# Optimization experiments

Hardware: AMD Instinct MI355X
Metric: run time of the kernel (lower is better)

The kernel has to match this reference:

```python
import jax, jax.numpy as jnp
import numpy as np

B, NT, NZ, NX, NREC = 4, 256, 192, 192, 128
DT, DH = 0.001, 10.0


def setup_inputs() -> dict:
    key = jax.random.key(0)
    k1, k2, k3, k4 = jax.random.split(key, 4)
    # source wavelets, one trace per shot
    x = jax.random.normal(k1, (B, NT, 1), dtype=jnp.float32) * 1e2
    # realistic elastic media
    vp = 2500.0 + 1000.0 * jax.random.uniform(k2, (NZ, NX), dtype=jnp.float32)
    vs = vp / 1.78
    rho = 2000.0 + 300.0 * jax.random.uniform(k3, (NZ, NX), dtype=jnp.float32)
    # per-shot source location (z=5 near surface, random x)
    src_x = jax.random.randint(k4, (B,), 10, NX - 10)
    src_loc = jnp.stack([jnp.full((B,), 5), src_x], axis=1).astype(jnp.int32)
    # receiver line at depth z=5
    rec_x = jnp.linspace(10, NX - 10, NREC).astype(jnp.int32)
    rec_loc = jnp.stack([jnp.full((NREC,), 5, dtype=jnp.int32), rec_x], axis=1)
    return {"x": x, "vp": vp, "vs": vs, "rho": rho,
            "src_loc": src_loc, "rec_loc": rec_loc}


# staggered-grid first differences (forward / backward), zero-padded at edges
def _dxf(f):
    return jnp.pad(jnp.diff(f, axis=-1), ((0, 0), (0, 0), (0, 1))) / DH

def _dxb(f):
    return jnp.pad(jnp.diff(f, axis=-1), ((0, 0), (0, 0), (1, 0))) / DH

def _dzf(f):
    return jnp.pad(jnp.diff(f, axis=-2), ((0, 0), (0, 1), (0, 0))) / DH

def _dzb(f):
    return jnp.pad(jnp.diff(f, axis=-2), ((0, 0), (1, 0), (0, 0))) / DH


def _propagate(x, vp, vs, rho, src_loc, rec_loc):
    lam = rho * (vp ** 2 - 2.0 * vs ** 2)
    mu = rho * vs ** 2
    lam2mu = lam + 2.0 * mu
    buoy = DT / rho  # buoyancy * dt
    bidx = jnp.arange(B)
    sz, sx = src_loc[:, 0], src_loc[:, 1]
    rz, rx = rec_loc[:, 0], rec_loc[:, 1]

    def step(carry, wav_t):
        vx, vz, txx, tzz, txz = carry
        # velocity update from stress divergence
        vx = vx + buoy * (_dxf(txx) + _dzb(txz))
        vz = vz + buoy * (_dxb(txz) + _dzf(tzz))
        # stress update from velocity gradients
        dvxdx = _dxb(vx)
        dvzdz = _dzb(vz)
        txx = txx + DT * (lam2mu * dvxdx + lam * dvzdz)
        tzz = tzz + DT * (lam * dvxdx + lam2mu * dvzdz)
        txz = txz + DT * mu * (_dzf(vx) + _dxf(vz))
        # explosive source injection into txx, tzz (source_type = ['txx','tzz'])
        txx = txx.at[bidx, sz, sx].add(wav_t)
        tzz = tzz.at[bidx, sz, sx].add(wav_t)
        # probe extraction: (B, NREC)
        return (vx, vz, txx, tzz, txz), (vx[:, rz, rx], vz[:, rz, rx])

    z = jnp.zeros((B, NZ, NX), dtype=vp.dtype)
    _, (rvx, rvz) = jax.lax.scan(step, (z, z, z, z, z), x[:, :, 0].T)
    # torch: stack(dim=1) -> (B,NT,NREC); permute(1,2,0) -> (NT,NREC,B); cat dim=2
    y_vx = jnp.transpose(rvx, (0, 2, 1))  # (NT, NREC, B)
    y_vz = jnp.transpose(rvz, (0, 2, 1))
    return jnp.concatenate([y_vx, y_vz], axis=2)  # (NT, NREC, 2B)


def reference(x, vp, vs, rho, src_loc, rec_loc):
    return _propagate(x, vp, vs, rho, src_loc, rec_loc)
```

## Files before the change

### kernel.cpp

```cpp
#include <hip/hip_runtime.h>

#pragma clang fp contract(off)

#define B_    4
#define NT_   256
#define NZ_   192
#define NX_   192
#define NREC_ 128
#define DT_   0.001f
#define DH_   10.0f

#define N_CELL  (NZ_ * NX_)
#define N_FIELD (B_ * N_CELL)

#define K_     4
#define ROWS   3
#define NTHR   1024
#define VH     (2 * K_ - 1)
#define SH     (2 * K_)
#define VROWS  (ROWS + 2 * VH)
#define SROWS  (ROWS + 2 * SH)
#define TILES  (NZ_ / ROWS)
#define NBLK   (B_ * TILES)
#define NX4    (NX_ / 4)
#define LDS_BYTES ((2 * VROWS + 3 * SROWS) * NX_ * 4)

using f4 = __attribute__((ext_vector_type(4))) float;

__global__ void mat_kernel(const float* __restrict__ vp, const float* __restrict__ vs,
                           const float* __restrict__ rho,
                           float* __restrict__ lam, float* __restrict__ dtmu,
                           float* __restrict__ lam2mu, float* __restrict__ buoy) {
    int i = blockIdx.x * blockDim.x + threadIdx.x;
    if (i >= N_CELL) return;
    float vpi = vp[i], vsi = vs[i], rhoi = rho[i];
    float vs2 = vsi * vsi;
    float mui = rhoi * vs2;
    float lami = rhoi * (vpi * vpi - 2.0f * vs2);
    lam[i] = lami;
    dtmu[i] = DT_ * mui;
    lam2mu[i] = lami + 2.0f * mui;
    buoy[i] = DT_ * (1.0f / rhoi);
    buoy[i] = DT_ / rhoi;
}

template<int S>
__device__ __forceinline__ void substep(
    bool zin, int z, int srow, int x4, int x0, int z0, int sz, int sx, int b, int t0,
    f4& r_vx, f4& r_vz, f4& r_txx, f4& r_tzz, f4& r_txz,
    const f4& m_bu, const f4& m_l, const f4& m_lm, const f4& m_dtm,
    float* __restrict__ vxl, float* __restrict__ vzl,
    float* __restrict__ txxl, float* __restrict__ tzzl, float* __restrict__ txzl,
    const float* __restrict__ wav,
    bool rec_ok, int rec_idx, int tid, float* __restrict__ out,
    int base, float* __restrict__ vxw, float* __restrict__ vzw,
    float* __restrict__ txxw, float* __restrict__ tzzw, float* __restrict__ txzw) {
    const int t = t0 + S;
    const int sOff = srow * NX_ + x0;
    const int vOff = (srow - 1) * NX_ + x0;

    {
        constexpr int hv = 2 * (K_ - 1 - S) + 1;
        bool act = zin && (z >= z0 - hv) && (z <= z0 + ROWS - 1 + hv);
        if (act) {
            f4 txn  = *reinterpret_cast<const f4*>(txxl + sOff + (x4 < NX4 - 1 ? 4 : 0));
            f4 tzp  = *reinterpret_cast<const f4*>(txzl + sOff - (x4 > 0 ? 4 : 0));
            f4 tzm  = *reinterpret_cast<const f4*>(txzl + sOff - NX_);
            f4 tzzp = *reinterpret_cast<const f4*>(tzzl + sOff + NX_);
#pragma unroll
            for (int e = 0; e < 4; ++e) {
                int xg = x0 + e;
                float txx_c = r_txx[e];
                float txxp1 = (e == 3) ? txn[0] : r_txx[e + 1];
                float txz_c = r_txz[e];
                float txzm1 = (e == 0) ? tzp[3] : r_txz[e - 1];
                float dxf_txx = (xg < NX_ - 1) ? (txxp1 - txx_c) / DH_ : 0.0f;
                float dzb_txz = (z >= 1)       ? (txz_c - tzm[e]) / DH_ : 0.0f;
                float dxb_txz = (xg >= 1)      ? (txz_c - txzm1) / DH_ : 0.0f;
                float dzf_tzz = (z < NZ_ - 1)  ? (tzzp[e] - r_tzz[e]) / DH_ : 0.0f;
                r_vx[e] = r_vx[e] + m_bu[e] * (dxf_txx + dzb_txz);
                r_vz[e] = r_vz[e] + m_bu[e] * (dxb_txz + dzf_tzz);
            }
            *reinterpret_cast<f4*>(vxl + vOff) = r_vx;
            *reinterpret_cast<f4*>(vzl + vOff) = r_vz;
            if (S == K_ - 1) {
                if (z >= z0 && z < z0 + ROWS) {
                    *reinterpret_cast<f4*>(vxw + base + z * NX_ + x0) = r_vx;
                    *reinterpret_cast<f4*>(vzw + base + z * NX_ + x0) = r_vz;
                }
            }
        }
    }
    __syncthreads();

    if (rec_ok) {
        size_t o = ((size_t)t * NREC_ + tid) * (2 * B_);
        out[o + b]      = vxl[rec_idx];
        out[o + B_ + b] = vzl[rec_idx];
    }

    {
        constexpr int hs = 2 * (K_ - 1 - S);
        bool act = zin && (z >= z0 - hs) && (z <= z0 + ROWS - 1 + hs);
        if (act) {
            f4 vxp  = *reinterpret_cast<const f4*>(vxl + vOff - (x4 > 0 ? 4 : 0));
            f4 vxzp = *reinterpret_cast<const f4*>(vxl + vOff + NX_);
            f4 vzn  = *reinterpret_cast<const f4*>(vzl + vOff + (x4 < NX4 - 1 ? 4 : 0));
            f4 vzm  = *reinterpret_cast<const f4*>(vzl + vOff - NX_);
            float w = wav[b * NT_ + t];
#pragma unroll
            for (int e = 0; e < 4; ++e) {
                int xg = x0 + e;
                float vx_c = r_vx[e];
                float vz_c = r_vz[e];
                float vxm1 = (e == 0) ? vxp[3] : r_vx[e - 1];
                float vzp1 = (e == 3) ? vzn[0] : r_vz[e + 1];
                float dvxdx  = (xg >= 1)      ? (vx_c - vxm1) / DH_ : 0.0f;
                float dvzdz  = (z >= 1)       ? (vz_c - vzm[e]) / DH_ : 0.0f;
                float dzf_vx = (z < NZ_ - 1)  ? (vxzp[e] - vx_c) / DH_ : 0.0f;
                float dxf_vz = (xg < NX_ - 1) ? (vzp1 - vz_c) / DH_ : 0.0f;
                float a  = r_txx[e] + DT_ * (m_lm[e] * dvxdx + m_l[e] * dvzdz);
                float bb = r_tzz[e] + DT_ * (m_l[e] * dvxdx + m_lm[e] * dvzdz);
                float cc = r_txz[e] + m_dtm[e] * (dzf_vx + dxf_vz);
                if (z == sz && xg == sx) { a = a + w; bb = bb + w; }
                r_txx[e] = a; r_tzz[e] = bb; r_txz[e] = cc;
            }
            *reinterpret_cast<f4*>(txxl + sOff) = r_txx;
            *reinterpret_cast<f4*>(tzzl + sOff) = r_tzz;
            *reinterpret_cast<f4*>(txzl + sOff) = r_txz;
            if (S == K_ - 1) {
                int g = base + z * NX_ + x0;
                *reinterpret_cast<f4*>(txxw + g) = r_txx;
                *reinterpret_cast<f4*>(tzzw + g) = r_tzz;
                *reinterpret_cast<f4*>(txzw + g) = r_txz;
            }
        }
    }
    __syncthreads();
}

__global__ void __launch_bounds__(NTHR, 4)
step_kernel(const float* __restrict__ vxr, const float* __restrict__ vzr,
            const float* __restrict__ txxr, const float* __restrict__ tzzr,
            const float* __restrict__ txzr,
            float* __restrict__ vxw, float* __restrict__ vzw,
            float* __restrict__ txxw, float* __restrict__ tzzw, float* __restrict__ txzw,
            const float* __restrict__ lam, const float* __restrict__ dtmu,
            const float* __restrict__ l2m, const float* __restrict__ buoy,
            const float* __restrict__ wav, int t0,
            const int* __restrict__ src_loc, const int* __restrict__ rec_loc,
            float* __restrict__ out) {
    extern __shared__ float smem[];
    float* __restrict__ vxl  = smem;
    float* __restrict__ vzl  = vxl  + VROWS * NX_;
    float* __restrict__ txxl = vzl  + VROWS * NX_;
    float* __restrict__ tzzl = txxl + SROWS * NX_;
    float* __restrict__ txzl = tzzl + SROWS * NX_;

    const int tid  = threadIdx.x;
    const int b    = blockIdx.x / TILES;
    const int tile = blockIdx.x % TILES;
    const int z0   = tile * ROWS;
    const int base = b * N_CELL;
    const int zv0  = z0 - VH;
    const int zs0  = z0 - SH;

    const int sz = src_loc[2 * b];
    const int sx = src_loc[2 * b + 1];

    const int srow = tid / NX4;
    const int x4   = tid - srow * NX4;
    const int x0   = x4 * 4;
    const int z    = zs0 + srow;
    const bool zin = (srow < SROWS) && (z >= 0) && (z < NZ_);
    const bool vin = zin && srow >= 1 && srow <= VROWS;

    bool rec_ok = false;
    int rec_idx = 0;
    if (tid < NREC_) {
        int rz = rec_loc[2 * tid];
        int rx = rec_loc[2 * tid + 1];
        if (rz >= z0 && rz < z0 + ROWS) {
            rec_ok = true;
            rec_idx = (rz - zv0) * NX_ + rx;
        }
    }

    f4 r_vx = {0,0,0,0}, r_vz = {0,0,0,0}, r_txx = {0,0,0,0}, r_tzz = {0,0,0,0}, r_txz = {0,0,0,0};
    f4 m_bu = {0,0,0,0}, m_l = {0,0,0,0}, m_lm = {0,0,0,0}, m_dtm = {0,0,0,0};
    if (zin) {
        int g = base + z * NX_ + x0;
        int c = z * NX_ + x0;
        r_txx = *reinterpret_cast<const f4*>(txxr + g);
        r_tzz = *reinterpret_cast<const f4*>(tzzr + g);
        r_txz = *reinterpret_cast<const f4*>(txzr + g);
        m_bu  = *reinterpret_cast<const f4*>(buoy + c);
        m_l   = *reinterpret_cast<const f4*>(lam  + c);
        m_lm  = *reinterpret_cast<const f4*>(l2m  + c);
        m_dtm = *reinterpret_cast<const f4*>(dtmu + c);
        int sOff = srow * NX_ + x0;
        *reinterpret_cast<f4*>(txxl + sOff) = r_txx;
        *reinterpret_cast<f4*>(tzzl + sOff) = r_tzz;
        *reinterpret_cast<f4*>(txzl + sOff) = r_txz;
        if (vin) {
            r_vx = *reinterpret_cast<const f4*>(vxr + g);
            r_vz = *reinterpret_cast<const f4*>(vzr + g);
            int vOff = (srow - 1) * NX_ + x0;
            *reinterpret_cast<f4*>(vxl + vOff) = r_vx;
            *reinterpret_cast<f4*>(vzl + vOff) = r_vz;
        }
    }
    __syncthreads();

    substep<0>(zin, z, srow, x4, x0, z0, sz, sx, b, t0, r_vx, r_vz, r_txx, r_tzz, r_txz,
               m_bu, m_l, m_lm, m_dtm, vxl, vzl, txxl, tzzl, txzl,
               wav, rec_ok, rec_idx, tid, out, base, vxw, vzw, txxw, tzzw, txzw);
    substep<1>(zin, z, srow, x4, x0, z0, sz, sx, b, t0, r_vx, r_vz, r_txx, r_tzz, r_txz,
               m_bu, m_l, m_lm, m_dtm, vxl, vzl, txxl, tzzl, txzl,
               wav, rec_ok, rec_idx, tid, out, base, vxw, vzw, txxw, tzzw, txzw);
    substep<2>(zin, z, srow, x4, x0, z0, sz, sx, b, t0, r_vx, r_vz, r_txx, r_tzz, r_txz,
               m_bu, m_l, m_lm, m_dtm, vxl, vzl, txxl, tzzl, txzl,
               wav, rec_ok, rec_idx, tid, out, base, vxw, vzw, txxw, tzzw, txzw);
    substep<3>(zin, z, srow, x4, x0, z0, sz, sx, b, t0, r_vx, r_vz, r_txx, r_tzz, r_txz,
               m_bu, m_l, m_lm, m_dtm, vxl, vzl, txxl, tzzl, txzl,
               wav, rec_ok, rec_idx, tid, out, base, vxw, vzw, txxw, tzzw, txzw);
}

extern "C" void kernel_launch(void* const* d_in, const int* in_sizes, int n_in,
                              void* d_out, int out_size, void* d_ws, size_t ws_size,
                              hipStream_t stream) {
    const float* xw      = (const float*)d_in[0];
    const float* vp      = (const float*)d_in[1];
    const float* vs      = (const float*)d_in[2];
    const float* rho     = (const float*)d_in[3];
    const int*   src_loc = (const int*)d_in[4];
    const int*   rec_loc = (const int*)d_in[5];
    float*       out     = (float*)d_out;

    float* ws = (float*)d_ws;
    float* vx[2]  = { ws + 0 * N_FIELD, ws + 1 * N_FIELD };
    float* vz[2]  = { ws + 2 * N_FIELD, ws + 3 * N_FIELD };
    float* txx[2] = { ws + 4 * N_FIELD, ws + 5 * N_FIELD };
    float* tzz[2] = { ws + 6 * N_FIELD, ws + 7 * N_FIELD };
    float* txz[2] = { ws + 8 * N_FIELD, ws + 9 * N_FIELD };
    float* lam    = ws + 10 * N_FIELD;
    float* dtmu   = lam + N_CELL;
    float* l2m    = dtmu + N_CELL;
    float* buoy   = l2m + N_CELL;

    hipMemsetAsync(d_ws, 0, (size_t)10 * N_FIELD * sizeof(float), stream);

    mat_kernel<<<(N_CELL + 255) / 256, 256, 0, stream>>>(vp, vs, rho, lam, dtmu, l2m, buoy);

    for (int L = 0; L < NT_ / K_; ++L) {
        int p = L & 1;
        step_kernel<<<NBLK, NTHR, LDS_BYTES, stream>>>(
            vx[p], vz[p], txx[p], tzz[p], txz[p],
            vx[1 - p], vz[1 - p], txx[1 - p], tzz[1 - p], txz[1 - p],
            lam, dtmu, l2m, buoy,
            xw, L * K_, src_loc, rec_loc, out);
    }
}
```

Measured before the change: 1.154 ms.

## Split temporal-blocked stencil tiles in x and remap workgroups across XCDs

Each z-tile is split into two x halves, each computed by a 512-thread block on a 17x112 window, with halo rows clamped to the domain instead of padded. The first substep reads its stress neighbours straight from global memory rather than staging them in LDS. Shared memory becomes static and much smaller, and block IDs are remapped so neighbouring tiles land on the same XCD for L2 locality. The aim is more blocks in flight and less LDS staging per launch, at the cost of extra redundant halo computation in x and a second global read of neighbour values.

```diff
diff --git a/kernel.cpp b/kernel.cpp
--- a/kernel.cpp
+++ b/kernel.cpp
@@ -15,17 +15,19 @@
 
 #define K_     4
 #define ROWS   3
-#define NTHR   1024
-#define VH     (2 * K_ - 1)
-#define SH     (2 * K_)
-#define VROWS  (ROWS + 2 * VH)
-#define SROWS  (ROWS + 2 * SH)
+#define NTHR   512
+#define WR     17
+#define W4     28
+#define WX     112
+#define CELLS4 (WR * W4)
 #define TILES  (NZ_ / ROWS)
-#define NBLK   (B_ * TILES)
-#define NX4    (NX_ / 4)
-#define LDS_BYTES ((2 * VROWS + 3 * SROWS) * NX_ * 4)
+#define NBLK   (B_ * TILES * 2)
+#define NXCD   8
 
 using f4 = __attribute__((ext_vector_type(4))) float;
+
+__device__ __forceinline__ f4 LD4(const float* p) { return *reinterpret_cast<const f4*>(p); }
+__device__ __forceinline__ void ST4(float* p, f4 v) { *reinterpret_cast<f4*>(p) = v; }
 
 __global__ void mat_kernel(const float* __restrict__ vp, const float* __restrict__ vs,
                            const float* __restrict__ rho,
@@ -40,33 +42,101 @@
     lam[i] = lami;
     dtmu[i] = DT_ * mui;
     lam2mu[i] = lami + 2.0f * mui;
-    buoy[i] = DT_ * (1.0f / rhoi);
     buoy[i] = DT_ / rhoi;
 }
 
-template<int S>
-__device__ __forceinline__ void substep(
-    bool zin, int z, int srow, int x4, int x0, int z0, int sz, int sx, int b, int t0,
-    f4& r_vx, f4& r_vz, f4& r_txx, f4& r_tzz, f4& r_txz,
-    const f4& m_bu, const f4& m_l, const f4& m_lm, const f4& m_dtm,
-    float* __restrict__ vxl, float* __restrict__ vzl,
-    float* __restrict__ txxl, float* __restrict__ tzzl, float* __restrict__ txzl,
-    const float* __restrict__ wav,
-    bool rec_ok, int rec_idx, int tid, float* __restrict__ out,
-    int base, float* __restrict__ vxw, float* __restrict__ vzw,
-    float* __restrict__ txxw, float* __restrict__ tzzw, float* __restrict__ txzw) {
-    const int t = t0 + S;
-    const int sOff = srow * NX_ + x0;
-    const int vOff = (srow - 1) * NX_ + x0;
-
-    {
-        constexpr int hv = 2 * (K_ - 1 - S) + 1;
-        bool act = zin && (z >= z0 - hv) && (z <= z0 + ROWS - 1 + hv);
+__global__ void __launch_bounds__(NTHR, 4)
+step_kernel(const float* __restrict__ vxr, const float* __restrict__ vzr,
+            const float* __restrict__ txxr, const float* __restrict__ tzzr,
+            const float* __restrict__ txzr,
+            float* __restrict__ vxw, float* __restrict__ vzw,
+            float* __restrict__ txxw, float* __restrict__ tzzw, float* __restrict__ txzw,
+            const float* __restrict__ lam, const float* __restrict__ dtmu,
+            const float* __restrict__ l2m, const float* __restrict__ buoy,
+            const float* __restrict__ wav, int t0,
+            const int* __restrict__ src_loc, const int* __restrict__ rec_loc,
+            float* __restrict__ out) {
+    __shared__ float vxl[WR * WX];
+    __shared__ float vzl[WR * WX];
+    __shared__ float txxl[WR * WX];
+    __shared__ float tzzl[WR * WX];
+    __shared__ float txzl[WR * WX];
+
+    const int tid  = threadIdx.x;
+    const int wg   = (blockIdx.x % NXCD) * (NBLK / NXCD) + blockIdx.x / NXCD;
+    const int half = wg & 1;
+    const int tile = (wg >> 1) & 63;
+    const int b    = wg >> 7;
+    const int z0   = tile * ROWS;
+    const int xL   = half * 80;
+    const int xa0  = half * 96;
+    int zvL = z0 - 7;
+    zvL = zvL < 0 ? 0 : (zvL > NZ_ - WR ? NZ_ - WR : zvL);
+    const int base = b * N_CELL;
+
+    const int sz = src_loc[2 * b];
+    const int sx = src_loc[2 * b + 1];
+
+    const bool act = tid < CELLS4;
+    const int rr = act ? (tid / W4) : 0;
+    const int qq = act ? (tid - (tid / W4) * W4) : 0;
+    const int z  = zvL + rr;
+    const int x0 = xL + 4 * qq;
+    const int lo = rr * WX + 4 * qq;
+    const int oXp = (qq < W4 - 1) ? 4 : 0;
+    const int oXm = (qq > 0) ? 4 : 0;
+    const int oZp = (rr < WR - 1) ? WX : 0;
+    const int oZm = (rr > 0) ? WX : 0;
+    const int g   = base + z * NX_ + x0;
+    const int c   = z * NX_ + x0;
+    const int gXp = g + ((x0 < NX_ - 4) ? 4 : 0);
+    const int gXm = g - ((x0 > 0) ? 4 : 0);
+    const int gZm = g - ((z > 0) ? NX_ : 0);
+    const int gZp = g + ((z < NZ_ - 1) ? NX_ : 0);
+    const bool owned = act && (z >= z0) && (z < z0 + ROWS) && (x0 >= xa0) && (x0 < xa0 + 96);
+
+    bool rec_ok = false;
+    int rec_idx = 0;
+    if (tid < NREC_) {
+        int rz = rec_loc[2 * tid];
+        int rx = rec_loc[2 * tid + 1];
+        if (rz >= z0 && rz < z0 + ROWS && rx >= xa0 && rx < xa0 + 96) {
+            rec_ok = true;
+            rec_idx = (rz - zvL) * WX + (rx - xL);
+        }
+    }
+
+    f4 r_vx = {0,0,0,0}, r_vz = {0,0,0,0}, r_txx = {0,0,0,0}, r_tzz = {0,0,0,0}, r_txz = {0,0,0,0};
+    f4 m_bu = {0,0,0,0}, m_l = {0,0,0,0}, m_lm = {0,0,0,0}, m_dtm = {0,0,0,0};
+    if (act) {
+        r_vx  = LD4(vxr + g);
+        r_vz  = LD4(vzr + g);
+        r_txx = LD4(txxr + g);
+        r_tzz = LD4(tzzr + g);
+        r_txz = LD4(txzr + g);
+        m_bu  = LD4(buoy + c);
+        m_l   = LD4(lam + c);
+        m_lm  = LD4(l2m + c);
+        m_dtm = LD4(dtmu + c);
+    }
+
+#pragma unroll
+    for (int s = 0; s < K_; ++s) {
+        const int t = t0 + s;
+
         if (act) {
-            f4 txn  = *reinterpret_cast<const f4*>(txxl + sOff + (x4 < NX4 - 1 ? 4 : 0));
-            f4 tzp  = *reinterpret_cast<const f4*>(txzl + sOff - (x4 > 0 ? 4 : 0));
-            f4 tzm  = *reinterpret_cast<const f4*>(txzl + sOff - NX_);
-            f4 tzzp = *reinterpret_cast<const f4*>(tzzl + sOff + NX_);
+            f4 txn, tzp, tzm, tzzp;
+            if (s == 0) {
+                txn  = LD4(txxr + gXp);
+                tzp  = LD4(txzr + gXm);
+                tzm  = LD4(txzr + gZm);
+                tzzp = LD4(tzzr + gZp);
+            } else {
+                txn  = LD4(txxl + lo + oXp);
+                tzp  = LD4(txzl + lo - oXm);
+                tzm  = LD4(txzl + lo - oZm);
+                tzzp = LD4(tzzl + lo + oZp);
+            }
 #pragma unroll
             for (int e = 0; e < 4; ++e) {
                 int xg = x0 + e;
@@ -81,32 +151,26 @@
                 r_vx[e] = r_vx[e] + m_bu[e] * (dxf_txx + dzb_txz);
                 r_vz[e] = r_vz[e] + m_bu[e] * (dxb_txz + dzf_tzz);
             }
-            *reinterpret_cast<f4*>(vxl + vOff) = r_vx;
-            *reinterpret_cast<f4*>(vzl + vOff) = r_vz;
-            if (S == K_ - 1) {
-                if (z >= z0 && z < z0 + ROWS) {
-                    *reinterpret_cast<f4*>(vxw + base + z * NX_ + x0) = r_vx;
-                    *reinterpret_cast<f4*>(vzw + base + z * NX_ + x0) = r_vz;
-                }
-            }
-        }
-    }
-    __syncthreads();
-
-    if (rec_ok) {
-        size_t o = ((size_t)t * NREC_ + tid) * (2 * B_);
-        out[o + b]      = vxl[rec_idx];
-        out[o + B_ + b] = vzl[rec_idx];
-    }
-
-    {
-        constexpr int hs = 2 * (K_ - 1 - S);
-        bool act = zin && (z >= z0 - hs) && (z <= z0 + ROWS - 1 + hs);
+            ST4(vxl + lo, r_vx);
+            ST4(vzl + lo, r_vz);
+            if (s == K_ - 1 && owned) {
+                ST4(vxw + g, r_vx);
+                ST4(vzw + g, r_vz);
+            }
+        }
+        __syncthreads();
+
+        if (rec_ok) {
+            size_t o = ((size_t)t * NREC_ + tid) * (2 * B_);
+            out[o + b]      = vxl[rec_idx];
+            out[o + B_ + b] = vzl[rec_idx];
+        }
+
         if (act) {
-            f4 vxp  = *reinterpret_cast<const f4*>(vxl + vOff - (x4 > 0 ? 4 : 0));
-            f4 vxzp = *reinterpret_cast<const f4*>(vxl + vOff + NX_);
-            f4 vzn  = *reinterpret_cast<const f4*>(vzl + vOff + (x4 < NX4 - 1 ? 4 : 0));
-            f4 vzm  = *reinterpret_cast<const f4*>(vzl + vOff - NX_);
+            f4 vxp  = LD4(vxl + lo - oXm);
+            f4 vxzp = LD4(vxl + lo + oZp);
+            f4 vzn  = LD4(vzl + lo + oXp);
+            f4 vzm  = LD4(vzl + lo - oZm);
             float w = wav[b * NT_ + t];
 #pragma unroll
             for (int e = 0; e < 4; ++e) {
@@ -125,105 +189,17 @@
                 if (z == sz && xg == sx) { a = a + w; bb = bb + w; }
                 r_txx[e] = a; r_tzz[e] = bb; r_txz[e] = cc;
             }
-            *reinterpret_cast<f4*>(txxl + sOff) = r_txx;
-            *reinterpret_cast<f4*>(tzzl + sOff) = r_tzz;
-            *reinterpret_cast<f4*>(txzl + sOff) = r_txz;
-            if (S == K_ - 1) {
-                int g = base + z * NX_ + x0;
-                *reinterpret_cast<f4*>(txxw + g) = r_txx;
-                *reinterpret_cast<f4*>(tzzw + g) = r_tzz;
-                *reinterpret_cast<f4*>(txzw + g) = r_txz;
-            }
-        }
-    }
-    __syncthreads();
-}
-
-__global__ void __launch_bounds__(NTHR, 4)
-step_kernel(const float* __restrict__ vxr, const float* __restrict__ vzr,
-            const float* __restrict__ txxr, const float* __restrict__ tzzr,
-            const float* __restrict__ txzr,
-            float* __restrict__ vxw, float* __restrict__ vzw,
-            float* __restrict__ txxw, float* __restrict__ tzzw, float* __restrict__ txzw,
-            const float* __restrict__ lam, const float* __restrict__ dtmu,
-            const float* __restrict__ l2m, const float* __restrict__ buoy,
-            const float* __restrict__ wav, int t0,
-            const int* __restrict__ src_loc, const int* __restrict__ rec_loc,
-            float* __restrict__ out) {
-    extern __shared__ float smem[];
-    float* __restrict__ vxl  = smem;
-    float* __restrict__ vzl  = vxl  + VROWS * NX_;
-    float* __restrict__ txxl = vzl  + VROWS * NX_;
-    float* __restrict__ tzzl = txxl + SROWS * NX_;
-    float* __restrict__ txzl = tzzl + SROWS * NX_;
-
-    const int tid  = threadIdx.x;
-    const int b    = blockIdx.x / TILES;
-    const int tile = blockIdx.x % TILES;
-    const int z0   = tile * ROWS;
-    const int base = b * N_CELL;
-    const int zv0  = z0 - VH;
-    const int zs0  = z0 - SH;
-
-    const int sz = src_loc[2 * b];
-    const int sx = src_loc[2 * b + 1];
-
-    const int srow = tid / NX4;
-    const int x4   = tid - srow * NX4;
-    const int x0   = x4 * 4;
-    const int z    = zs0 + srow;
-    const bool zin = (srow < SROWS) && (z >= 0) && (z < NZ_);
-    const bool vin = zin && srow >= 1 && srow <= VROWS;
-
-    bool rec_ok = false;
-    int rec_idx = 0;
-    if (tid < NREC_) {
-        int rz = rec_loc[2 * tid];
-        int rx = rec_loc[2 * tid + 1];
-        if (rz >= z0 && rz < z0 + ROWS) {
-            rec_ok = true;
-            rec_idx = (rz - zv0) * NX_ + rx;
-        }
-    }
-
-    f4 r_vx = {0,0,0,0}, r_vz = {0,0,0,0}, r_txx = {0,0,0,0}, r_tzz = {0,0,0,0}, r_txz = {0,0,0,0};
-    f4 m_bu = {0,0,0,0}, m_l = {0,0,0,0}, m_lm = {0,0,0,0}, m_dtm = {0,0,0,0};
-    if (zin) {
-        int g = base + z * NX_ + x0;
-        int c = z * NX_ + x0;
-        r_txx = *reinterpret_cast<const f4*>(txxr + g);
-        r_tzz = *reinterpret_cast<const f4*>(tzzr + g);
-        r_txz = *reinterpret_cast<const f4*>(txzr + g);
-        m_bu  = *reinterpret_cast<const f4*>(buoy + c);
-        m_l   = *reinterpret_cast<const f4*>(lam  + c);
-        m_lm  = *reinterpret_cast<const f4*>(l2m  + c);
-        m_dtm = *reinterpret_cast<const f4*>(dtmu + c);
-        int sOff = srow * NX_ + x0;
-        *reinterpret_cast<f4*>(txxl + sOff) = r_txx;
-        *reinterpret_cast<f4*>(tzzl + sOff) = r_tzz;
-        *reinterpret_cast<f4*>(txzl + sOff) = r_txz;
-        if (vin) {
-            r_vx = *reinterpret_cast<const f4*>(vxr + g);
-            r_vz = *reinterpret_cast<const f4*>(vzr + g);
-            int vOff = (srow - 1) * NX_ + x0;
-            *reinterpret_cast<f4*>(vxl + vOff) = r_vx;
-            *reinterpret_cast<f4*>(vzl + vOff) = r_vz;
-        }
-    }
-    __syncthreads();
-
-    substep<0>(zin, z, srow, x4, x0, z0, sz, sx, b, t0, r_vx, r_vz, r_txx, r_tzz, r_txz,
-               m_bu, m_l, m_lm, m_dtm, vxl, vzl, txxl, tzzl, txzl,
-               wav, rec_ok, rec_idx, tid, out, base, vxw, vzw, txxw, tzzw, txzw);
-    substep<1>(zin, z, srow, x4, x0, z0, sz, sx, b, t0, r_vx, r_vz, r_txx, r_tzz, r_txz,
-               m_bu, m_l, m_lm, m_dtm, vxl, vzl, txxl, tzzl, txzl,
-               wav, rec_ok, rec_idx, tid, out, base, vxw, vzw, txxw, tzzw, txzw);
-    substep<2>(zin, z, srow, x4, x0, z0, sz, sx, b, t0, r_vx, r_vz, r_txx, r_tzz, r_txz,
-               m_bu, m_l, m_lm, m_dtm, vxl, vzl, txxl, tzzl, txzl,
-               wav, rec_ok, rec_idx, tid, out, base, vxw, vzw, txxw, tzzw, txzw);
-    substep<3>(zin, z, srow, x4, x0, z0, sz, sx, b, t0, r_vx, r_vz, r_txx, r_tzz, r_txz,
-               m_bu, m_l, m_lm, m_dtm, vxl, vzl, txxl, tzzl, txzl,
-               wav, rec_ok, rec_idx, tid, out, base, vxw, vzw, txxw, tzzw, txzw);
+            ST4(txxl + lo, r_txx);
+            ST4(tzzl + lo, r_tzz);
+            ST4(txzl + lo, r_txz);
+            if (s == K_ - 1 && owned) {
+                ST4(txxw + g, r_txx);
+                ST4(tzzw + g, r_tzz);
+                ST4(txzw + g, r_txz);
+            }
+        }
+        __syncthreads();
+    }
 }
 
 extern "C" void kernel_launch(void* const* d_in, const int* in_sizes, int n_in,
@@ -254,7 +230,7 @@
 
     for (int L = 0; L < NT_ / K_; ++L) {
         int p = L & 1;
-        step_kernel<<<NBLK, NTHR, LDS_BYTES, stream>>>(
+        step_kernel<<<NBLK, NTHR, 0, stream>>>(
             vx[p], vz[p], txx[p], tzz[p], txz[p],
             vx[1 - p], vz[1 - p], txx[1 - p], tzz[1 - p], txz[1 - p],
             lam, dtmu, l2m, buoy,
```

After: 1.211 ms. 1.05x slower.
